# Kernel tuning notes

Measured on AMD Instinct MI355X. Metric: run time of the kernel, lower is better.

Reference implementation:

```python
import jax, jax.numpy as jnp
import numpy as np

K = 16          # hard-coded in FCM.forward
TEMPERATURE = 1.0  # init kwarg t
EPS = 1e-12     # torch F.normalize eps


def setup_inputs() -> dict:
    key = jax.random.key(0)
    N, D = 8192, 256
    feats = jax.random.normal(key, (N, D), dtype=jnp.float32)
    return {"feats": feats}


def reference(feats):
    N = feats.shape[0]
    # similarity scores (temperature = 1)
    scores = jnp.matmul(feats, feats.T) / TEMPERATURE  # [N, N]

    # squared euclidean pairwise distances (monotonic in cdist -> same topk indices)
    sq = jnp.sum(feats * feats, axis=1)  # [N]
    d2 = sq[:, None] + sq[None, :] - 2.0 * scores * TEMPERATURE
    # smallest k+1 distances -> largest k+1 of -d2
    _, idx = jax.lax.top_k(-d2, K + 1)  # [N, K+1]
    knn = idx[:, 1:K + 1]               # drop self, [N, K]

    # knn membership matrix: M[i, j] = True iff j in knn(i)
    rows = jnp.arange(N)[:, None]
    M = jnp.zeros((N, N), dtype=bool).at[rows, knn].set(True)
    mutual = M & M.T  # mutual kNN

    # mask: -inf everywhere, 1.0 on the diagonal, scores at mutual-kNN entries
    eye = jnp.eye(N, dtype=bool)
    mask = jnp.where(eye, jnp.float32(1.0), -jnp.inf)
    mask = jnp.where(mutual, scores, mask)

    attn = jax.nn.softmax(mask, axis=-1)       # rows always have finite diag
    feats_fcm = feats + jnp.matmul(attn, feats)

    # L2 normalize rows (torch F.normalize semantics: x / max(||x||, eps))
    norm = jnp.linalg.norm(feats_fcm, axis=1, keepdims=True)
    return feats_fcm / jnp.maximum(norm, EPS)
```

## Files before the change

### kernel.cpp

```cpp
#include <hip/hip_runtime.h>
#include <math.h>

#define NPTS 8192
#define DIM  256
#define NSLOT 17
#define CAP  256
#define LCAP 48
#define RSEL 24
#define ZTH  (-2.45f)
typedef unsigned int uint;
typedef unsigned short ushort;
typedef unsigned long long ull;
typedef __attribute__((ext_vector_type(8))) short bf16x8;
typedef __attribute__((ext_vector_type(4))) float f32x4;

__device__ __forceinline__ ushort f2bf(float f) {
    uint x = __float_as_uint(f);
    return (ushort)((x + 0x7fffu + ((x >> 16) & 1u)) >> 16);
}

__global__ void pack_kernel(const float* __restrict__ feats, ushort* __restrict__ fbp,
                            float* __restrict__ sq, double* __restrict__ sqd,
                            int* __restrict__ cnt_g) {
    const int cb = (blockIdx.x * 128 + threadIdx.x) >> 6;
    const int l  = threadIdx.x & 63;
    const int l15 = l & 15, lg = l >> 4;
    const float* src = feats + (size_t)(cb * 16 + l15) * DIM + lg * 8;
    ushort* dst = fbp + (size_t)cb * 4096 + l * 8;
    double pd = 0.0;
#pragma unroll
    for (int kb = 0; kb < 8; ++kb) {
        const float4 v0 = *reinterpret_cast<const float4*>(src + kb * 32);
        const float4 v1 = *reinterpret_cast<const float4*>(src + kb * 32 + 4);
        pd += (double)v0.x * v0.x + (double)v0.y * v0.y +
              (double)v0.z * v0.z + (double)v0.w * v0.w;
        pd += (double)v1.x * v1.x + (double)v1.y * v1.y +
              (double)v1.z * v1.z + (double)v1.w * v1.w;
        bf16x8 bv;
        bv[0] = (short)f2bf(v0.x); bv[1] = (short)f2bf(v0.y);
        bv[2] = (short)f2bf(v0.z); bv[3] = (short)f2bf(v0.w);
        bv[4] = (short)f2bf(v1.x); bv[5] = (short)f2bf(v1.y);
        bv[6] = (short)f2bf(v1.z); bv[7] = (short)f2bf(v1.w);
        *reinterpret_cast<bf16x8*>(dst + kb * 512) = bv;
    }
    pd += __shfl_xor(pd, 16, 64);
    pd += __shfl_xor(pd, 32, 64);
    if (lg == 0) {
        const int row = cb * 16 + l15;
        sq[row] = (float)pd; sqd[row] = pd; cnt_g[row] = 0;
    }
}

__global__ void stats_kernel(const float* __restrict__ sq, float* __restrict__ musig) {
    __shared__ double s0s[16], s1s[16];
    const int t = threadIdx.x, lane = t & 63, w = t >> 6;
    double s0 = 0.0, s1 = 0.0;
    for (int r = t; r < NPTS; r += 1024) {
        const double v = (double)sq[r];
        s0 += v; s1 += v * v;
    }
#pragma unroll
    for (int off = 32; off > 0; off >>= 1) {
        s0 += __shfl_down(s0, off, 64);
        s1 += __shfl_down(s1, off, 64);
    }
    if (lane == 0) { s0s[w] = s0; s1s[w] = s1; }
    __syncthreads();
    if (t == 0) {
        double a0 = 0.0, a1 = 0.0;
#pragma unroll
        for (int q = 0; q < 16; ++q) { a0 += s0s[q]; a1 += s1s[q]; }
        const double mu = a0 / NPTS;
        const double var = a1 / NPTS - mu * mu;
        musig[0] = (float)mu;
        musig[1] = (float)fmax(var, 1.0);
    }
}

__global__ __launch_bounds__(512, 2) void gemm_select_kernel(
    const ushort* __restrict__ fbp, const float* __restrict__ sq,
    const float* __restrict__ musig, int* __restrict__ cand, int* __restrict__ cnt_g) {
    __shared__ ushort As[16384];
    __shared__ int    cbuf[64][LCAP];
    __shared__ float  Ts[64], sqi_s[64];
    __shared__ int    cnt[64];
    __shared__ int    base_s[64], n_s[64];

    const int tid = threadIdx.x;
    const int w   = tid >> 6;
    const int l   = tid & 63;
    const int l15 = l & 15, lg = l >> 4;
    const int rowblk = (blockIdx.x >> 3) * 2 + (blockIdx.x & 1);
    const int row0   = rowblk * 64;
    const int Jbase  = ((blockIdx.x & 7) >> 1) * 2048;

    if (tid < 64) {
        const float mu  = musig[0];
        const float var = musig[1];
        const float qi  = sq[row0 + tid];
        sqi_s[tid] = qi;
        Ts[tid]    = qi + mu + ZTH * sqrtf(var + 4.f * qi);
        cnt[tid]   = 0;
    }
    {
        const ushort* src = fbp + (size_t)(row0 >> 4) * 4096;
#pragma unroll
        for (int s = 0; s < 4; ++s) {
            const int idx = tid + s * 512;
            *reinterpret_cast<bf16x8*>(As + idx * 8) =
                *reinterpret_cast<const bf16x8*>(src + (size_t)idx * 8);
        }
    }
    __syncthreads();

    const int gcol = w * 32;
    const ushort* bp = fbp + (size_t)((Jbase >> 4) + w * 2) * 4096 + l * 8;

    bf16x8 bb[2][2];
#pragma unroll
    for (int cf = 0; cf < 2; ++cf) {
        bb[0][cf] = *reinterpret_cast<const bf16x8*>(bp + cf * 4096);
        bb[1][cf] = *reinterpret_cast<const bf16x8*>(bp + cf * 4096 + 512);
    }

    for (int tile = 0; tile < 8; ++tile) {
        f32x4 acc[4][2];
#pragma unroll
        for (int mf = 0; mf < 4; ++mf) {
            acc[mf][0] = (f32x4){0.f, 0.f, 0.f, 0.f};
            acc[mf][1] = (f32x4){0.f, 0.f, 0.f, 0.f};
        }
#pragma unroll
        for (int ks = 0; ks < 8; ++ks) {
            const int cur = ks & 1;
            bf16x8 af[4];
#pragma unroll
            for (int mf = 0; mf < 4; ++mf)
                af[mf] = *reinterpret_cast<const bf16x8*>(
                    As + ((mf * 8 + ks) * 64 + l) * 8);
#pragma unroll
            for (int mf = 0; mf < 4; ++mf) {
                acc[mf][0] = __builtin_amdgcn_mfma_f32_16x16x32_bf16(af[mf], bb[cur][0], acc[mf][0], 0, 0, 0);
                acc[mf][1] = __builtin_amdgcn_mfma_f32_16x16x32_bf16(af[mf], bb[cur][1], acc[mf][1], 0, 0, 0);
            }
            if (tile < 7 || ks < 6) {
                const int ntile = (ks >= 6) ? tile + 1 : tile;
                const int nks   = (ks + 2) & 7;
#pragma unroll
                for (int cf = 0; cf < 2; ++cf)
                    bb[cur][cf] = *reinterpret_cast<const bf16x8*>(
                        bp + (size_t)ntile * 65536 + cf * 4096 + nks * 512);
            }
        }
        const int Jt = Jbase + tile * 256;
        float sqc[2];
#pragma unroll
        for (int cf = 0; cf < 2; ++cf) sqc[cf] = sq[Jt + gcol + cf * 16 + l15];
#pragma unroll
        for (int mf = 0; mf < 4; ++mf)
#pragma unroll
            for (int cf = 0; cf < 2; ++cf)
#pragma unroll
                for (int r = 0; r < 4; ++r) {
                    const int row = mf * 16 + lg * 4 + r;
                    const float tt = Ts[row];
                    const float key = sqi_s[row] + sqc[cf] - 2.f * acc[mf][cf][r];
                    if (key < tt) {
                        const int kq2 = min((int)((tt - key) * 4096.f), 524287);
                        const uint val = ((uint)max(kq2, 0) << 13) |
                                         (uint)(Jt + gcol + cf * 16 + l15);
                        const int pos = atomicAdd(&cnt[row], 1);
                        if (pos < LCAP) cbuf[row][pos] = (int)val;
                    }
                }
    }
    __syncthreads();
    if (tid < 64) {
        const int local = cnt[tid];
        const int n = min(local, LCAP);
        const int add = (local > LCAP) ? (n + (1 << 20)) : n;
        base_s[tid] = atomicAdd(&cnt_g[row0 + tid], add);
        n_s[tid] = n;
    }
    __syncthreads();
    for (int s = tid; s < 64 * LCAP; s += 512) {
        const int r = s / LCAP, k2 = s - r * LCAP;
        if (k2 < n_s[r]) {
            const int b = base_s[r] + k2;
            if (b < CAP) cand[(size_t)(row0 + r) * CAP + b] = cbuf[r][k2];
        }
    }
}

__global__ void fallback_kernel(const float* __restrict__ feats, const float* __restrict__ sq,
                                int* __restrict__ cand, int* __restrict__ cnt_g) {
    __shared__ float fi_s[DIM];
    __shared__ float keys[NPTS];
    __shared__ float rkey[4];
    __shared__ int   rid[4];
    __shared__ int   badlist[256];
    __shared__ int   nbad_s;
    const int t = threadIdx.x;
    if (t == 0) nbad_s = 0;
    __syncthreads();
    {
        const int myrow = blockIdx.x * 256 + t;
        const int v = cnt_g[myrow];
        if (v < NSLOT || v > CAP) badlist[atomicAdd(&nbad_s, 1)] = myrow;
    }
    __syncthreads();
    const int nb = nbad_s;
    for (int bi = 0; bi < nb; ++bi) {
        const int row = badlist[bi];
        fi_s[t] = feats[(size_t)row * DIM + t];
        __syncthreads();
        const float sqi = sq[row];
        for (int p = 0; p < NPTS / 256; ++p) {
            const int jj = p * 256 + t;
            const float* fj = feats + (size_t)jj * DIM;
            float d = 0.f;
            for (int dq = 0; dq < DIM / 4; ++dq) {
                const float4 b4 = *reinterpret_cast<const float4*>(fj + dq * 4);
                const float4 a4 = *reinterpret_cast<const float4*>(&fi_s[dq * 4]);
                d = fmaf(a4.x, b4.x, fmaf(a4.y, b4.y, fmaf(a4.z, b4.z, fmaf(a4.w, b4.w, d))));
            }
            keys[jj] = sqi + sq[jj] - 2.f * d;
        }
        __syncthreads();
        for (int r = 0; r < 64; ++r) {
            float bk = INFINITY; int bj = 0x7fffffff;
            for (int p = 0; p < NPTS / 256; ++p) {
                const int jj = p * 256 + t;
                const float kv = keys[jj];
                if (kv < bk || (kv == bk && jj < bj)) { bk = kv; bj = jj; }
            }
#pragma unroll
            for (int off = 1; off <= 32; off <<= 1) {
                const float ok = __shfl_xor(bk, off, 64);
                const int   oj = __shfl_xor(bj, off, 64);
                if (ok < bk || (ok == bk && oj < bj)) { bk = ok; bj = oj; }
            }
            if ((t & 63) == 0) { rkey[t >> 6] = bk; rid[t >> 6] = bj; }
            __syncthreads();
            float fk = rkey[0]; int fj2 = rid[0];
#pragma unroll
            for (int q = 1; q < 4; ++q)
                if (rkey[q] < fk || (rkey[q] == fk && rid[q] < fj2)) { fk = rkey[q]; fj2 = rid[q]; }
            if (t == 0) {
                cand[(size_t)row * CAP + r] = (int)(((uint)(524287 - r) << 13) | (uint)fj2);
                keys[fj2] = INFINITY;
            }
            __syncthreads();
        }
        if (t == 0) cnt_g[row] = 64;
        __syncthreads();
    }
}

__global__ __launch_bounds__(256) void refine_kernel(
    const float* __restrict__ feats, const double* __restrict__ sqd,
    const int* __restrict__ cand, const int* __restrict__ cnt_g,
    int* __restrict__ fidx, float* __restrict__ fscr) {
    __shared__ float fi_s[4][DIM];
    __shared__ int   sel_s[4][RSEL];
    const int w = threadIdx.x >> 6, l = threadIdx.x & 63;
    const int i = blockIdx.x * 4 + w;
    *reinterpret_cast<float4*>(&fi_s[w][l * 4]) =
        *reinterpret_cast<const float4*>(feats + (size_t)i * DIM + l * 4);
    __syncthreads();
    const int nc   = min(cnt_g[i], CAP);
    const int want = min(nc, RSEL);
    const int* crow = cand + (size_t)i * CAP;
    uint pk[4]; bool act[4];
#pragma unroll
    for (int b = 0; b < 4; ++b) {
        const int c = b * 64 + l;
        act[b] = (c < nc);
        pk[b]  = act[b] ? (uint)crow[c] : 0u;
    }
    uint lo = 0u, hi = 0xffffffffu;
    while (lo < hi) {
        const uint mid = (uint)(((ull)lo + (ull)hi + 1ULL) >> 1);
        int c = 0;
#pragma unroll
        for (int b = 0; b < 4; ++b) c += __popcll(__ballot(act[b] && pk[b] >= mid));
        if (c >= want) lo = mid; else hi = mid - 1u;
    }
    {
        int base = 0;
#pragma unroll
        for (int b = 0; b < 4; ++b) {
            const bool s = act[b] && pk[b] >= lo;
            const ull bal = __ballot(s);
            const int pos = base + __popcll(bal & ((1ULL << l) - 1ULL));
            if (s && pos < RSEL) sel_s[w][pos] = (int)(pk[b] & 8191u);
            base += __popcll(bal);
        }
    }
    const int  cidx = l >> 1, half = l & 1;
    const bool mine = (cidx < want);
    const int  j    = mine ? sel_s[w][cidx] : i;
    double dot0 = 0.0, dot1 = 0.0;
    if (mine) {
        const float* fj = feats + (size_t)j * DIM + half * 128;
        const float* fi = &fi_s[w][half * 128];
#pragma unroll 8
        for (int dq = 0; dq < 16; ++dq) {
            const float4 a0 = *reinterpret_cast<const float4*>(fi + dq * 8);
            const float4 a1 = *reinterpret_cast<const float4*>(fi + dq * 8 + 4);
            const float4 b0 = *reinterpret_cast<const float4*>(fj + dq * 8);
            const float4 b1 = *reinterpret_cast<const float4*>(fj + dq * 8 + 4);
            dot0 += (double)a0.x * b0.x + (double)a0.y * b0.y +
                    (double)a0.z * b0.z + (double)a0.w * b0.w;
            dot1 += (double)a1.x * b1.x + (double)a1.y * b1.y +
                    (double)a1.z * b1.z + (double)a1.w * b1.w;
        }
    }
    double dot = dot0 + dot1;
    dot += __shfl_xor(dot, 1, 64);
    const double dd = sqd[i] + sqd[j] - 2.0 * dot;
    const ull key = (mine && half == 0)
                        ? ((ull)(__double_as_longlong(fmax(dd, 0.0)) & ~8191LL) | (ull)(uint)j)
                        : ~0ULL;
    ull klo = 0ULL, khi = 0x4330000000000000ULL;
    while (klo < khi) {
        const ull mid = klo + ((khi - klo) >> 1);
        const int c = __popcll(__ballot(key <= mid));
        if (c >= NSLOT) khi = mid; else klo = mid + 1ULL;
    }
    const bool s2 = (key <= khi);
    const ull bal = __ballot(s2);
    const int pos = __popcll(bal & ((1ULL << l) - 1ULL));
    if (s2 && pos < NSLOT) {
        fidx[(size_t)i * NSLOT + pos] = j;
        fscr[(size_t)i * NSLOT + pos] = (float)dot;
    }
}

__global__ void fcm_out_kernel(const float* __restrict__ feats,
                               const int* __restrict__ knn_idx,
                               const float* __restrict__ knn_scr,
                               float* __restrict__ out) {
    const int w    = threadIdx.x >> 6;
    const int lane = threadIdx.x & 63;
    const int i    = blockIdx.x * 4 + w;

    int jt = -1; float st = 0.f; bool valid = false;
    if (lane < NSLOT) {
        jt = knn_idx[(size_t)i * NSLOT + lane];
        st = knn_scr[(size_t)i * NSLOT + lane];
        if (jt != i) {
            const int* nb = knn_idx + (size_t)jt * NSLOT;
#pragma unroll
            for (int s = 0; s < NSLOT; ++s) valid |= (nb[s] == i);
        }
    }
    float val = valid ? st : -INFINITY;
#pragma unroll
    for (int off = 32; off > 0; off >>= 1) val = fmaxf(val, __shfl_xor(val, off, 64));
    const float m  = fmaxf(1.0f, val);
    const float wt = valid ? expf(st - m) : 0.f;
    float ws = wt;
#pragma unroll
    for (int off = 32; off > 0; off >>= 1) ws += __shfl_xor(ws, off, 64);
    const float wdiag = expf(1.0f - m);
    const float inv   = 1.0f / (ws + wdiag);

    const float4 fi = *reinterpret_cast<const float4*>(feats + (size_t)i * DIM + lane * 4);
    float ax = fi.x * wdiag, ay = fi.y * wdiag, az = fi.z * wdiag, aw = fi.w * wdiag;
    for (int t = 0; t < NSLOT; ++t) {
        const float wtt = __shfl(wt, t, 64);
        const int   jj  = __shfl(jt, t, 64);
        if (wtt > 0.f) {
            const float4 fj = *reinterpret_cast<const float4*>(feats + (size_t)jj * DIM + lane * 4);
            ax = fmaf(wtt, fj.x, ax); ay = fmaf(wtt, fj.y, ay);
            az = fmaf(wtt, fj.z, az); aw = fmaf(wtt, fj.w, aw);
        }
    }
    const float ox = fmaf(ax, inv, fi.x), oy = fmaf(ay, inv, fi.y);
    const float oz = fmaf(az, inv, fi.z), ow = fmaf(aw, inv, fi.w);
    float nn = ox * ox + oy * oy + oz * oz + ow * ow;
#pragma unroll
    for (int off = 32; off > 0; off >>= 1) nn += __shfl_xor(nn, off, 64);
    const float scl = 1.0f / fmaxf(sqrtf(nn), 1e-12f);
    float4 o; o.x = ox * scl; o.y = oy * scl; o.z = oz * scl; o.w = ow * scl;
    *reinterpret_cast<float4*>(out + (size_t)i * DIM + lane * 4) = o;
}

extern "C" void kernel_launch(void* const* d_in, const int* in_sizes, int n_in,
                              void* d_out, int out_size, void* d_ws, size_t ws_size,
                              hipStream_t stream) {
    (void)in_sizes; (void)n_in; (void)out_size; (void)ws_size;
    const float* feats = (const float*)d_in[0];
    float* out = (float*)d_out;
    char* ws = (char*)d_ws;
    size_t off = 0;
    float*  sq    = (float*) (ws + off); off += NPTS * 4;
    double* sqd   = (double*)(ws + off); off += NPTS * 8;
    float*  musig = (float*) (ws + off); off += 128;
    ushort* fbp   = (ushort*)(ws + off); off += (size_t)NPTS * DIM * 2;
    int*    cand  = (int*)   (ws + off); off += (size_t)NPTS * CAP * 4;
    int*    cnt_g = (int*)   (ws + off); off += NPTS * 4;
    int*    fidx  = (int*)   (ws + off); off += NPTS * NSLOT * 4;
    float*  fscr  = (float*) (ws + off); off += NPTS * NSLOT * 4;

    pack_kernel<<<NPTS / 32, 128, 0, stream>>>(feats, fbp, sq, sqd, cnt_g);
    stats_kernel<<<1, 1024, 0, stream>>>(sq, musig);
    gemm_select_kernel<<<(NPTS / 64) * 4, 512, 0, stream>>>(fbp, sq, musig, cand, cnt_g);
    fallback_kernel<<<NPTS / 256, 256, 0, stream>>>(feats, sq, cand, cnt_g);
    refine_kernel<<<NPTS / 4, 256, 0, stream>>>(feats, sqd, cand, cnt_g, fidx, fscr);
    fcm_out_kernel<<<NPTS / 4, 256, 0, stream>>>(feats, fidx, fscr, out);
}
```

Baseline: 112.6 us.

## Switch Gram GEMM to 32x32x16 MFMA with matching packed layout

Repacks the bf16 feature buffer into 32-row blocks laid out for the 32x32x16 bf16 MFMA. The select GEMM now issues two 32x32 MFMAs per k-step instead of eight 16x16 ones, with fewer LDS A-fragment reads and B-fragment loads. The epilogue is remapped to the 32x32 accumulator layout. This cuts instruction and load overhead per FLOP, but a wave now blocks on fewer, longer MFMAs, and the pack kernel runs with smaller 64-thread blocks.

Measured after the change: 123.3 us. +9.5%, slower.

```diff
diff --git a/kernel.cpp b/kernel.cpp
--- a/kernel.cpp
+++ b/kernel.cpp
@@ -13,6 +13,7 @@
 typedef unsigned long long ull;
 typedef __attribute__((ext_vector_type(8))) short bf16x8;
 typedef __attribute__((ext_vector_type(4))) float f32x4;
+typedef __attribute__((ext_vector_type(16))) float f32x16;
 
 __device__ __forceinline__ ushort f2bf(float f) {
     uint x = __float_as_uint(f);
@@ -22,16 +23,17 @@
 __global__ void pack_kernel(const float* __restrict__ feats, ushort* __restrict__ fbp,
                             float* __restrict__ sq, double* __restrict__ sqd,
                             int* __restrict__ cnt_g) {
-    const int cb = (blockIdx.x * 128 + threadIdx.x) >> 6;
-    const int l  = threadIdx.x & 63;
-    const int l15 = l & 15, lg = l >> 4;
-    const float* src = feats + (size_t)(cb * 16 + l15) * DIM + lg * 8;
-    ushort* dst = fbp + (size_t)cb * 4096 + l * 8;
+    const int cb = blockIdx.x;
+    const int l  = threadIdx.x;
+    const int row = cb * 32 + (l & 31);
+    const int kh  = (l >> 5) * 8;
+    const float* src = feats + (size_t)row * DIM + kh;
+    ushort* dst = fbp + (size_t)cb * 8192 + l * 8;
     double pd = 0.0;
 #pragma unroll
-    for (int kb = 0; kb < 8; ++kb) {
-        const float4 v0 = *reinterpret_cast<const float4*>(src + kb * 32);
-        const float4 v1 = *reinterpret_cast<const float4*>(src + kb * 32 + 4);
+    for (int kb = 0; kb < 16; ++kb) {
+        const float4 v0 = *reinterpret_cast<const float4*>(src + kb * 16);
+        const float4 v1 = *reinterpret_cast<const float4*>(src + kb * 16 + 4);
         pd += (double)v0.x * v0.x + (double)v0.y * v0.y +
               (double)v0.z * v0.z + (double)v0.w * v0.w;
         pd += (double)v1.x * v1.x + (double)v1.y * v1.y +
@@ -43,10 +45,8 @@
         bv[6] = (short)f2bf(v1.z); bv[7] = (short)f2bf(v1.w);
         *reinterpret_cast<bf16x8*>(dst + kb * 512) = bv;
     }
-    pd += __shfl_xor(pd, 16, 64);
     pd += __shfl_xor(pd, 32, 64);
-    if (lg == 0) {
-        const int row = cb * 16 + l15;
+    if (l < 32) {
         sq[row] = (float)pd; sqd[row] = pd; cnt_g[row] = 0;
     }
 }
@@ -89,7 +89,7 @@
     const int tid = threadIdx.x;
     const int w   = tid >> 6;
     const int l   = tid & 63;
-    const int l15 = l & 15, lg = l >> 4;
+    const int l31 = l & 31, lh = l >> 5;
     const int rowblk = (blockIdx.x >> 3) * 2 + (blockIdx.x & 1);
     const int row0   = rowblk * 64;
     const int Jbase  = ((blockIdx.x & 7) >> 1) * 2048;
@@ -103,7 +103,7 @@
         cnt[tid]   = 0;
     }
     {
-        const ushort* src = fbp + (size_t)(row0 >> 4) * 4096;
+        const ushort* src = fbp + (size_t)(row0 >> 5) * 8192;
 #pragma unroll
         for (int s = 0; s < 4; ++s) {
             const int idx = tid + s * 512;
@@ -114,65 +114,46 @@
     __syncthreads();
 
     const int gcol = w * 32;
-    const ushort* bp = fbp + (size_t)((Jbase >> 4) + w * 2) * 4096 + l * 8;
-
-    bf16x8 bb[2][2];
-#pragma unroll
-    for (int cf = 0; cf < 2; ++cf) {
-        bb[0][cf] = *reinterpret_cast<const bf16x8*>(bp + cf * 4096);
-        bb[1][cf] = *reinterpret_cast<const bf16x8*>(bp + cf * 4096 + 512);
-    }
+    const ushort* bp = fbp + (size_t)((Jbase >> 5) + w) * 8192 + l * 8;
+
+    bf16x8 bb[2];
+    bb[0] = *reinterpret_cast<const bf16x8*>(bp);
+    bb[1] = *reinterpret_cast<const bf16x8*>(bp + 512);
 
     for (int tile = 0; tile < 8; ++tile) {
-        f32x4 acc[4][2];
-#pragma unroll
-        for (int mf = 0; mf < 4; ++mf) {
-            acc[mf][0] = (f32x4){0.f, 0.f, 0.f, 0.f};
-            acc[mf][1] = (f32x4){0.f, 0.f, 0.f, 0.f};
-        }
-#pragma unroll
-        for (int ks = 0; ks < 8; ++ks) {
-            const int cur = ks & 1;
-            bf16x8 af[4];
-#pragma unroll
-            for (int mf = 0; mf < 4; ++mf)
-                af[mf] = *reinterpret_cast<const bf16x8*>(
-                    As + ((mf * 8 + ks) * 64 + l) * 8);
-#pragma unroll
-            for (int mf = 0; mf < 4; ++mf) {
-                acc[mf][0] = __builtin_amdgcn_mfma_f32_16x16x32_bf16(af[mf], bb[cur][0], acc[mf][0], 0, 0, 0);
-                acc[mf][1] = __builtin_amdgcn_mfma_f32_16x16x32_bf16(af[mf], bb[cur][1], acc[mf][1], 0, 0, 0);
-            }
-            if (tile < 7 || ks < 6) {
-                const int ntile = (ks >= 6) ? tile + 1 : tile;
-                const int nks   = (ks + 2) & 7;
-#pragma unroll
-                for (int cf = 0; cf < 2; ++cf)
-                    bb[cur][cf] = *reinterpret_cast<const bf16x8*>(
-                        bp + (size_t)ntile * 65536 + cf * 4096 + nks * 512);
+        f32x16 acc[2];
+        acc[0] = (f32x16)(0.f);
+        acc[1] = (f32x16)(0.f);
+#pragma unroll
+        for (int kb = 0; kb < 16; ++kb) {
+            const int cur = kb & 1;
+            const bf16x8 af0 = *reinterpret_cast<const bf16x8*>(As + (kb * 512 + l * 8));
+            const bf16x8 af1 = *reinterpret_cast<const bf16x8*>(As + (8192 + kb * 512 + l * 8));
+            acc[0] = __builtin_amdgcn_mfma_f32_32x32x16_bf16(af0, bb[cur], acc[0], 0, 0, 0);
+            acc[1] = __builtin_amdgcn_mfma_f32_32x32x16_bf16(af1, bb[cur], acc[1], 0, 0, 0);
+            if (tile < 7 || kb < 14) {
+                const int c2 = tile * 16 + kb + 2;
+                bb[cur] = *reinterpret_cast<const bf16x8*>(
+                    bp + (size_t)(c2 >> 4) * 65536 + (c2 & 15) * 512);
             }
         }
         const int Jt = Jbase + tile * 256;
-        float sqc[2];
-#pragma unroll
-        for (int cf = 0; cf < 2; ++cf) sqc[cf] = sq[Jt + gcol + cf * 16 + l15];
-#pragma unroll
-        for (int mf = 0; mf < 4; ++mf)
-#pragma unroll
-            for (int cf = 0; cf < 2; ++cf)
-#pragma unroll
-                for (int r = 0; r < 4; ++r) {
-                    const int row = mf * 16 + lg * 4 + r;
-                    const float tt = Ts[row];
-                    const float key = sqi_s[row] + sqc[cf] - 2.f * acc[mf][cf][r];
-                    if (key < tt) {
-                        const int kq2 = min((int)((tt - key) * 4096.f), 524287);
-                        const uint val = ((uint)max(kq2, 0) << 13) |
-                                         (uint)(Jt + gcol + cf * 16 + l15);
-                        const int pos = atomicAdd(&cnt[row], 1);
-                        if (pos < LCAP) cbuf[row][pos] = (int)val;
-                    }
+        const int colg = Jt + gcol + l31;
+        const float sqc = sq[colg];
+#pragma unroll
+        for (int mf = 0; mf < 2; ++mf)
+#pragma unroll
+            for (int r = 0; r < 16; ++r) {
+                const int row = mf * 32 + (r & 3) + 8 * (r >> 2) + 4 * lh;
+                const float tt = Ts[row];
+                const float key = sqi_s[row] + sqc - 2.f * acc[mf][r];
+                if (key < tt) {
+                    const int kq2 = min((int)((tt - key) * 4096.f), 524287);
+                    const uint val = ((uint)max(kq2, 0) << 13) | (uint)colg;
+                    const int pos = atomicAdd(&cnt[row], 1);
+                    if (pos < LCAP) cbuf[row][pos] = (int)val;
                 }
+            }
     }
     __syncthreads();
     if (tid < 64) {
@@ -404,7 +385,7 @@
     int*    fidx  = (int*)   (ws + off); off += NPTS * NSLOT * 4;
     float*  fscr  = (float*) (ws + off); off += NPTS * NSLOT * 4;
 
-    pack_kernel<<<NPTS / 32, 128, 0, stream>>>(feats, fbp, sq, sqd, cnt_g);
+    pack_kernel<<<NPTS / 32, 64, 0, stream>>>(feats, fbp, sq, sqd, cnt_g);
     stats_kernel<<<1, 1024, 0, stream>>>(sq, musig);
     gemm_select_kernel<<<(NPTS / 64) * 4, 512, 0, stream>>>(fbp, sq, musig, cand, cnt_g);
     fallback_kernel<<<NPTS / 256, 256, 0, stream>>>(feats, sq, cand, cnt_g);
```
